# Optimization experiments

Hardware: AMD Instinct MI355X
Metric: run time of the kernel (lower is better)

## Reference

```python
import jax, jax.numpy as jnp
import numpy as np

BETA = 0.25  # commitment loss weight (init kwarg)


def setup_inputs() -> dict:
    key = jax.random.key(0)
    k1, k2 = jax.random.split(key)
    x = jax.random.normal(k1, (64, 32, 32, 64), dtype=jnp.float32)  # [B,H,W,D]
    # keras random_uniform_initializer default: U(-0.05, 0.05)
    embeddings = jax.random.uniform(k2, (64, 512), dtype=jnp.float32,
                                    minval=-0.05, maxval=0.05)  # [D,K]
    return {"x": x, "embeddings": embeddings}


def reference(x, embeddings):
    D, K = embeddings.shape
    flat = x.reshape(-1, D)  # [N,D]
    # squared L2 distances to each code: ||f||^2 + ||e||^2 - 2 f.e  -> [N,K]
    distances = (jnp.sum(flat * flat, axis=1, keepdims=True)
                 + jnp.sum(embeddings * embeddings, axis=0)
                 - 2.0 * (flat @ embeddings))
    idx = jnp.argmin(distances, axis=1)  # [N]
    # one-hot @ embeddings^T == gather of codebook rows
    quantized = jnp.take(embeddings.T, idx, axis=0).reshape(x.shape)
    commitment_loss = BETA * jnp.mean(jnp.square(jax.lax.stop_gradient(quantized) - x))
    codebook_loss = jnp.mean(jnp.square(quantized - jax.lax.stop_gradient(x)))
    loss = commitment_loss + codebook_loss
    # straight-through estimator
    out = x + jax.lax.stop_gradient(quantized - x)
    return out, loss
```

## Files before the change

### kernel.cpp

```cpp
#include <hip/hip_runtime.h>


#define N_ROWS 65536
#define DIM 64
#define KCODES 512
#define ROWS_PER_BLOCK 64
#define THREADS 512

typedef short s16x8 __attribute__((ext_vector_type(8)));
typedef float f32x4 __attribute__((ext_vector_type(4)));

#define LOSS_OFF   0
#define EN2_OFF    256
#define EN2B_OFF   2304
#define ET_OFF     4352
#define AFR_OFF    135424

#define TAU 1.2e-3f

__device__ __forceinline__ unsigned short f2bf(float f) {
    unsigned u = __float_as_uint(f);
    return (unsigned short)((u + 0x7fffu + ((u >> 16) & 1u)) >> 16);
}
__device__ __forceinline__ float bf2f(unsigned short h) {
    return __uint_as_float(((unsigned)h) << 16);
}
__device__ __forceinline__ void cvt8v(const float4 v0, const float4 v1,
                                      s16x8& hi, s16x8& lo) {
    const float vv[8] = {v0.x, v0.y, v0.z, v0.w, v1.x, v1.y, v1.z, v1.w};
    #pragma unroll
    for (int j = 0; j < 8; ++j) {
        const unsigned short h = f2bf(vv[j]);
        hi[j] = (short)h;
        lo[j] = (short)f2bf(vv[j] - bf2f(h));
    }
}

__global__ void vq_prep(const float* __restrict__ emb, char* __restrict__ ws) {
    const int k = blockIdx.x * 256 + threadIdx.x;
    if (k == 0) *(double*)(ws + LOSS_OFF) = 0.0;
    float* en2  = (float*)(ws + EN2_OFF);
    float* en2b = (float*)(ws + EN2B_OFF);
    float* eT   = (float*)(ws + ET_OFF);
    uint4* Afr  = (uint4*)(ws + AFR_OFF);
    const int ctg = k >> 4, c = k & 15;
    float s = 0.0f;
    #pragma unroll
    for (int ks = 0; ks < 2; ++ks) {
        #pragma unroll
        for (int g = 0; g < 4; ++g) {
            unsigned short hb[8], lb[8];
            #pragma unroll
            for (int j = 0; j < 8; ++j) {
                const int d = ks * 32 + g * 8 + j;
                const float v = emb[d * KCODES + k];
                eT[k * DIM + d] = v;
                s = fmaf(v, v, s);
                const unsigned short h = f2bf(v);
                hb[j] = h;
                lb[j] = f2bf(v - bf2f(h));
            }
            uint4 H, L;
            H.x = hb[0] | ((unsigned)hb[1] << 16); H.y = hb[2] | ((unsigned)hb[3] << 16);
            H.z = hb[4] | ((unsigned)hb[5] << 16); H.w = hb[6] | ((unsigned)hb[7] << 16);
            L.x = lb[0] | ((unsigned)lb[1] << 16); L.y = lb[2] | ((unsigned)lb[3] << 16);
            L.z = lb[4] | ((unsigned)lb[5] << 16); L.w = lb[6] | ((unsigned)lb[7] << 16);
            const int lane = g * 16 + c;
            Afr[((ctg * 2 + ks) * 2 + 0) * 64 + lane] = H;
            Afr[((ctg * 2 + ks) * 2 + 1) * 64 + lane] = L;
        }
    }
    en2[k] = s;
    en2b[k] = s + 6.0f;
}

__global__ __launch_bounds__(THREADS, 2)
void vq_main(const float* __restrict__ x, const char* __restrict__ ws,
             float* __restrict__ out, double* __restrict__ loss_acc) {
    __shared__ float xs[ROWS_PER_BLOCK][DIM];
    __shared__ s16x8 Bfr[4][2][2][64];
    __shared__ unsigned long long sm_all[4][8][16];
    __shared__ unsigned pick[ROWS_PER_BLOCK];
    __shared__ unsigned char llist[ROWS_PER_BLOCK];
    __shared__ unsigned long long wmin[8];
    __shared__ double lpart[8];
    __shared__ int lcnt;

    const int tid = threadIdx.x;
    const int bid = blockIdx.x;
    const int w = __builtin_amdgcn_readfirstlane(tid >> 6);
    const int l = tid & 63;
    if (tid == 0) lcnt = 0;

    {
        const int r_abs = tid >> 3;
        const int jg    = tid & 7;
        const float* p = x + (size_t)(bid * ROWS_PER_BLOCK + r_abs) * DIM + jg * 8;
        const float4 v0 = *(const float4*)p;
        const float4 v1 = *(const float4*)(p + 4);
        *(float4*)&xs[r_abs][jg * 8]     = v0;
        *(float4*)&xs[r_abs][jg * 8 + 4] = v1;
        s16x8 h, lo;
        cvt8v(v0, v1, h, lo);
        const int rt = r_abs >> 4, c = r_abs & 15;
        Bfr[rt][jg >> 2][0][(jg & 3) * 16 + c] = h;
        Bfr[rt][jg >> 2][1][(jg & 3) * 16 + c] = lo;
    }

    const s16x8* Afr = (const s16x8*)(ws + AFR_OFF);
    s16x8 Aeh[4][2], Ael[4][2];
    #pragma unroll
    for (int ct = 0; ct < 4; ++ct) {
        #pragma unroll
        for (int ks = 0; ks < 2; ++ks) {
            const int ctg = w * 4 + ct;
            Aeh[ct][ks] = Afr[((ctg * 2 + ks) * 2 + 0) * 64 + l];
            Ael[ct][ks] = Afr[((ctg * 2 + ks) * 2 + 1) * 64 + l];
        }
    }
    const float* en2b = (const float*)(ws + EN2B_OFF);
    f32x4 enf[4];
    #pragma unroll
    for (int ct = 0; ct < 4; ++ct) {
        const float4 t = *(const float4*)(en2b + w * 64 + ct * 16 + (l >> 4) * 4);
        enf[ct][0] = t.x; enf[ct][1] = t.y; enf[ct][2] = t.z; enf[ct][3] = t.w;
    }
    const int codebase = w * 64 + (l >> 4) * 4;

    __syncthreads();

    #pragma unroll 2
    for (int bt = 0; bt < 4; ++bt) {
        const s16x8 bh0 = Bfr[bt][0][0][l];
        const s16x8 bl0 = Bfr[bt][0][1][l];
        const s16x8 bh1 = Bfr[bt][1][0][l];
        const s16x8 bl1 = Bfr[bt][1][1][l];

        unsigned m1 = 0xFFFFFFFFu, m2 = 0xFFFFFFFFu;
        #pragma unroll
        for (int ct = 0; ct < 4; ++ct) {
            f32x4 a = {0.f, 0.f, 0.f, 0.f};
            a = __builtin_amdgcn_mfma_f32_16x16x32_bf16(Aeh[ct][0], bh0, a, 0, 0, 0);
            a = __builtin_amdgcn_mfma_f32_16x16x32_bf16(Aeh[ct][1], bh1, a, 0, 0, 0);
            a = __builtin_amdgcn_mfma_f32_16x16x32_bf16(Ael[ct][0], bh0, a, 0, 0, 0);
            a = __builtin_amdgcn_mfma_f32_16x16x32_bf16(Ael[ct][1], bh1, a, 0, 0, 0);
            a = __builtin_amdgcn_mfma_f32_16x16x32_bf16(Aeh[ct][0], bl0, a, 0, 0, 0);
            a = __builtin_amdgcn_mfma_f32_16x16x32_bf16(Aeh[ct][1], bl1, a, 0, 0, 0);
            #pragma unroll
            for (int rg = 0; rg < 4; ++rg) {
                const float m = fmaf(-2.0f, a[rg], enf[ct][rg]);
                const unsigned u = (__float_as_uint(m) & 0xFFFFFE00u)
                                 | (unsigned)(codebase + ct * 16 + rg);
                const unsigned hi = m1 > u ? m1 : u;
                m1 = m1 < u ? m1 : u;
                m2 = m2 < hi ? m2 : hi;
            }
        }
        #pragma unroll
        for (int mask = 16; mask <= 32; mask <<= 1) {
            const unsigned o1 = __shfl_xor(m1, mask);
            const unsigned o2 = __shfl_xor(m2, mask);
            const unsigned hi  = m1 > o1 ? m1 : o1;
            const unsigned lo2 = m2 < o2 ? m2 : o2;
            m1 = m1 < o1 ? m1 : o1;
            m2 = hi < lo2 ? hi : lo2;
        }
        if (l < 16) sm_all[bt][w][l] = ((unsigned long long)m1 << 32) | m2;
    }
    __syncthreads();

    if (tid < ROWS_PER_BLOCK) {
        const int bt = tid >> 4, c = tid & 15;
        unsigned long long p = sm_all[bt][0][c];
        unsigned m1 = (unsigned)(p >> 32), m2 = (unsigned)p;
        #pragma unroll
        for (int w2 = 1; w2 < 8; ++w2) {
            p = sm_all[bt][w2][c];
            const unsigned a1 = (unsigned)(p >> 32), a2 = (unsigned)p;
            const unsigned hi  = m1 > a1 ? m1 : a1;
            const unsigned lo2 = m2 < a2 ? m2 : a2;
            m1 = m1 < a1 ? m1 : a1;
            m2 = hi < lo2 ? hi : lo2;
        }
        pick[tid] = m1 & 0x1FFu;
        const float f1 = __uint_as_float(m1 & 0xFFFFFE00u);
        const float f2 = __uint_as_float(m2 & 0xFFFFFE00u);
        if (f2 - f1 < TAU) {
            const int i = atomicAdd(&lcnt, 1);
            llist[i] = (unsigned char)tid;
        }
    }
    __syncthreads();

    {
        const float* eT  = (const float*)(ws + ET_OFF);
        const float* en2 = (const float*)(ws + EN2_OFF);
        const int nfb = lcnt;
        for (int i = 0; i < nfb; ++i) {
            const int r = llist[i];
            const float4* fr = (const float4*)xs[r];

            float4 a4 = make_float4(0.f, 0.f, 0.f, 0.f);
            #pragma unroll
            for (int j = 0; j < 16; ++j) {
                const float4 f = fr[j];
                a4.x = fmaf(f.x, f.x, a4.x);
                a4.y = fmaf(f.y, f.y, a4.y);
                a4.z = fmaf(f.z, f.z, a4.z);
                a4.w = fmaf(f.w, f.w, a4.w);
            }
            const float r2 = (a4.x + a4.y) + (a4.z + a4.w);

            const int k = tid;
            const float4* ek = (const float4*)(eT + k * DIM);
            float4 acc4 = make_float4(0.f, 0.f, 0.f, 0.f);
            #pragma unroll
            for (int j = 0; j < 16; ++j) {
                const float4 e = ek[j];
                const float4 f = fr[j];
                acc4.x = fmaf(f.x, e.x, acc4.x);
                acc4.y = fmaf(f.y, e.y, acc4.y);
                acc4.z = fmaf(f.z, e.z, acc4.z);
                acc4.w = fmaf(f.w, e.w, acc4.w);
            }
            const float dot = (acc4.x + acc4.y) + (acc4.z + acc4.w);
            const float s = (r2 + en2[k]) - 2.0f * dot;
            unsigned long long best =
                ((unsigned long long)__float_as_uint(s) << 32) | (unsigned)k;
            #pragma unroll
            for (int mask = 1; mask <= 32; mask <<= 1) {
                const unsigned long long o = __shfl_xor(best, mask);
                if (o < best) best = o;
            }
            if (l == 0) wmin[w] = best;
            __syncthreads();
            if (tid == 0) {
                unsigned long long b = wmin[0];
                #pragma unroll
                for (int t = 1; t < 8; ++t) if (wmin[t] < b) b = wmin[t];
                pick[r] = (unsigned)(b & 0x1FFu);
            }
            __syncthreads();
        }
    }
    __syncthreads();

    {
        const float* eT = (const float*)(ws + ET_OFF);
        const int r = tid >> 3, g8 = tid & 7;
        const int grow = bid * ROWS_PER_BLOCK + r;
        const float4* xr = (const float4*)&xs[r][g8 * 8];
        const float4* qr = (const float4*)(eT + pick[r] * DIM) + g8 * 2;
        float4* orow = ((float4*)out) + (size_t)grow * 16 + g8 * 2;
        float lsum = 0.0f;
        #pragma unroll
        for (int j = 0; j < 2; ++j) {
            const float4 q = qr[j], xv = xr[j];
            float4 o; float dx;
            dx = q.x - xv.x; o.x = xv.x + dx; lsum = fmaf(dx, dx, lsum);
            dx = q.y - xv.y; o.y = xv.y + dx; lsum = fmaf(dx, dx, lsum);
            dx = q.z - xv.z; o.z = xv.z + dx; lsum = fmaf(dx, dx, lsum);
            dx = q.w - xv.w; o.w = xv.w + dx; lsum = fmaf(dx, dx, lsum);
            orow[j] = o;
        }
        double dl = (double)lsum;
        #pragma unroll
        for (int off = 32; off > 0; off >>= 1) dl += __shfl_down(dl, off);
        if (l == 0) lpart[w] = dl;
    }
    __syncthreads();
    if (tid == 0) {
        double s = lpart[0];
        #pragma unroll
        for (int t = 1; t < 8; ++t) s += lpart[t];
        atomicAdd(loss_acc, s);
    }
}

__global__ void vq_fin(const double* __restrict__ loss_acc, float* __restrict__ out) {
    if (threadIdx.x == 0)
        out[N_ROWS * DIM] = (float)(1.25 * loss_acc[0] * (1.0 / (double)(N_ROWS * DIM)));
}

extern "C" void kernel_launch(void* const* d_in, const int* in_sizes, int n_in,
                              void* d_out, int out_size, void* d_ws, size_t ws_size,
                              hipStream_t stream) {
    const float* x   = (const float*)d_in[0];
    const float* emb = (const float*)d_in[1];
    float* out = (float*)d_out;
    char*  ws  = (char*)d_ws;

    vq_prep<<<2, 256, 0, stream>>>(emb, ws);
    vq_main<<<N_ROWS / ROWS_PER_BLOCK, THREADS, 0, stream>>>(
        x, ws, out, (double*)(ws + LOSS_OFF));
    vq_fin<<<1, 1, 0, stream>>>((const double*)(ws + LOSS_OFF), out);
}
```

Baseline: 50.13 us.

## Replace atomic loss accumulation with per-block slots, tree argmin, padded x tile

Each block now writes its partial loss to its own workspace slot instead of doing a double atomicAdd, and the final kernel reduces the 1024 slots in parallel with 512 threads. This also removes the need to zero the accumulator in the prep kernel. The per-lane top-two argmin is restructured from a serial chain of 16 compare-updates into a pairwise tree to shorten the dependency chain. The shared x tile is padded to 68 floats per row to reduce LDS bank conflicts, at the cost of slightly more shared memory.

```diff
diff --git a/kernel.cpp b/kernel.cpp
--- a/kernel.cpp
+++ b/kernel.cpp
@@ -6,15 +6,16 @@
 #define KCODES 512
 #define ROWS_PER_BLOCK 64
 #define THREADS 512
+#define XPAD 68
 
 typedef short s16x8 __attribute__((ext_vector_type(8)));
 typedef float f32x4 __attribute__((ext_vector_type(4)));
 
-#define LOSS_OFF   0
-#define EN2_OFF    256
-#define EN2B_OFF   2304
-#define ET_OFF     4352
-#define AFR_OFF    135424
+#define LSLOT_OFF  0
+#define EN2_OFF    8192
+#define EN2B_OFF   10240
+#define ET_OFF     12288
+#define AFR_OFF    143360
 
 #define TAU 1.2e-3f
 
@@ -38,7 +39,6 @@
 
 __global__ void vq_prep(const float* __restrict__ emb, char* __restrict__ ws) {
     const int k = blockIdx.x * 256 + threadIdx.x;
-    if (k == 0) *(double*)(ws + LOSS_OFF) = 0.0;
     float* en2  = (float*)(ws + EN2_OFF);
     float* en2b = (float*)(ws + EN2B_OFF);
     float* eT   = (float*)(ws + ET_OFF);
@@ -75,9 +75,9 @@
 }
 
 __global__ __launch_bounds__(THREADS, 2)
-void vq_main(const float* __restrict__ x, const char* __restrict__ ws,
-             float* __restrict__ out, double* __restrict__ loss_acc) {
-    __shared__ float xs[ROWS_PER_BLOCK][DIM];
+void vq_main(const float* __restrict__ x, char* __restrict__ ws,
+             float* __restrict__ out) {
+    __shared__ float xs[ROWS_PER_BLOCK][XPAD];
     __shared__ s16x8 Bfr[4][2][2][64];
     __shared__ unsigned long long sm_all[4][8][16];
     __shared__ unsigned pick[ROWS_PER_BLOCK];
@@ -136,7 +136,7 @@
         const s16x8 bh1 = Bfr[bt][1][0][l];
         const s16x8 bl1 = Bfr[bt][1][1][l];
 
-        unsigned m1 = 0xFFFFFFFFu, m2 = 0xFFFFFFFFu;
+        unsigned uu[16];
         #pragma unroll
         for (int ct = 0; ct < 4; ++ct) {
             f32x4 a = {0.f, 0.f, 0.f, 0.f};
@@ -149,13 +149,30 @@
             #pragma unroll
             for (int rg = 0; rg < 4; ++rg) {
                 const float m = fmaf(-2.0f, a[rg], enf[ct][rg]);
-                const unsigned u = (__float_as_uint(m) & 0xFFFFFE00u)
-                                 | (unsigned)(codebase + ct * 16 + rg);
-                const unsigned hi = m1 > u ? m1 : u;
-                m1 = m1 < u ? m1 : u;
-                m2 = m2 < hi ? m2 : hi;
-            }
-        }
+                uu[ct * 4 + rg] = (__float_as_uint(m) & 0xFFFFFE00u)
+                                | (unsigned)(codebase + ct * 16 + rg);
+            }
+        }
+        unsigned b1[8], b2[8];
+        #pragma unroll
+        for (int i = 0; i < 8; ++i) {
+            const unsigned u = uu[2 * i], v = uu[2 * i + 1];
+            b1[i] = u < v ? u : v;
+            b2[i] = u < v ? v : u;
+        }
+        #pragma unroll
+        for (int st = 4; st > 0; st >>= 1) {
+            #pragma unroll
+            for (int i = 0; i < st; ++i) {
+                const unsigned x1 = b1[i], y1 = b1[i + st];
+                const unsigned lo = x1 < y1 ? x1 : y1;
+                const unsigned hi = x1 < y1 ? y1 : x1;
+                const unsigned s2 = b2[i] < b2[i + st] ? b2[i] : b2[i + st];
+                b1[i] = lo;
+                b2[i] = s2 < hi ? s2 : hi;
+            }
+        }
+        unsigned m1 = b1[0], m2 = b2[0];
         #pragma unroll
         for (int mask = 16; mask <= 32; mask <<= 1) {
             const unsigned o1 = __shfl_xor(m1, mask);
@@ -273,13 +290,25 @@
         double s = lpart[0];
         #pragma unroll
         for (int t = 1; t < 8; ++t) s += lpart[t];
-        atomicAdd(loss_acc, s);
-    }
-}
-
-__global__ void vq_fin(const double* __restrict__ loss_acc, float* __restrict__ out) {
-    if (threadIdx.x == 0)
-        out[N_ROWS * DIM] = (float)(1.25 * loss_acc[0] * (1.0 / (double)(N_ROWS * DIM)));
+        ((double*)(ws + LSLOT_OFF))[bid] = s;
+    }
+}
+
+__global__ __launch_bounds__(512)
+void vq_fin(const double* __restrict__ slots, float* __restrict__ out) {
+    __shared__ double sp[8];
+    const int tid = threadIdx.x;
+    double s = slots[tid] + slots[tid + 512];
+    #pragma unroll
+    for (int off = 32; off > 0; off >>= 1) s += __shfl_down(s, off);
+    if ((tid & 63) == 0) sp[tid >> 6] = s;
+    __syncthreads();
+    if (tid == 0) {
+        double t = sp[0];
+        #pragma unroll
+        for (int i = 1; i < 8; ++i) t += sp[i];
+        out[N_ROWS * DIM] = (float)(1.25 * t * (1.0 / (double)(N_ROWS * DIM)));
+    }
 }
 
 extern "C" void kernel_launch(void* const* d_in, const int* in_sizes, int n_in,
@@ -291,7 +320,6 @@
     char*  ws  = (char*)d_ws;
 
     vq_prep<<<2, 256, 0, stream>>>(emb, ws);
-    vq_main<<<N_ROWS / ROWS_PER_BLOCK, THREADS, 0, stream>>>(
-        x, ws, out, (double*)(ws + LOSS_OFF));
-    vq_fin<<<1, 1, 0, stream>>>((const double*)(ws + LOSS_OFF), out);
-}
+    vq_main<<<N_ROWS / ROWS_PER_BLOCK, THREADS, 0, stream>>>(x, ws, out);
+    vq_fin<<<1, 512, 0, stream>>>((const double*)(ws + LSLOT_OFF), out);
+}
```

After: 59.71 us. 1.19x slower.
